# Kernel tuning notes

Measured on AMD Instinct MI355X. Metric: run time of the kernel, lower is better.

## Reference

```python
import jax, jax.numpy as jnp
import numpy as np
import math

DIM = 1024
HEADS = 16
DIM_HEAD = 64
INNER = HEADS * DIM_HEAD
NUM_BUCKETS = 32
MAX_DISTANCE = 128


def setup_inputs() -> dict:
    key = jax.random.key(0)
    ks = jax.random.split(key, 6)
    x = jax.random.normal(ks[0], (2, 2048, DIM), dtype=jnp.float32)
    Wq = jax.random.normal(ks[1], (DIM, INNER), dtype=jnp.float32) * (DIM ** -0.5)
    Wkv = jax.random.normal(ks[2], (DIM, 2 * DIM_HEAD), dtype=jnp.float32) * (DIM ** -0.5)
    Wout = jax.random.normal(ks[3], (INNER, DIM), dtype=jnp.float32) * (INNER ** -0.5)
    bout = jnp.zeros((DIM,), dtype=jnp.float32)
    rel_emb = jax.random.normal(ks[4], (NUM_BUCKETS, HEADS), dtype=jnp.float32) * 0.02
    return {"x": x, "Wq": Wq, "Wkv": Wkv, "Wout": Wout, "bout": bout, "rel_emb": rel_emb}


def _relative_position_bucket(rel_pos, num_buckets=NUM_BUCKETS, max_distance=MAX_DISTANCE):
    # rel_pos: [i, j] int32, k_pos - q_pos
    n = jnp.maximum(-rel_pos, 0)
    max_exact = num_buckets // 2
    is_small = n < max_exact
    n_safe = jnp.maximum(n, 1)  # avoid log(0); masked by is_small anyway
    val_if_large = max_exact + (
        jnp.log(n_safe.astype(jnp.float32) / max_exact)
        / math.log(max_distance / max_exact)
        * (num_buckets - max_exact)
    ).astype(jnp.int32)
    val_if_large = jnp.minimum(val_if_large, num_buckets - 1)
    return jnp.where(is_small, n, val_if_large)


def reference(x, Wq, Wkv, Wout, bout, rel_emb):
    b, n, _ = x.shape
    scale = DIM_HEAD ** -0.5
    bias_scale = DIM_HEAD ** 0.5

    q = (x @ Wq).reshape(b, n, HEADS, DIM_HEAD).transpose(0, 2, 1, 3) * scale  # [b,h,n,d]
    kv = x @ Wkv  # [b,n,2d]
    k, v = kv[..., :DIM_HEAD], kv[..., DIM_HEAD:]  # shared single-head K/V [b,n,d]

    sim = jnp.einsum('bhid,bjd->bhij', q, k)

    # T5 relative position bias
    pos = jnp.arange(n, dtype=jnp.int32)
    rel_pos = pos[None, :] - pos[:, None]  # [i,j] = k_pos - q_pos
    rp_bucket = _relative_position_bucket(rel_pos)
    bias = rel_emb[rp_bucket]  # [i,j,h]
    sim = sim + jnp.transpose(bias, (2, 0, 1))[None] * bias_scale

    # causal mask: mask strictly-upper triangle
    causal_mask = jnp.triu(jnp.ones((n, n), dtype=bool), k=1)
    neg = jnp.finfo(sim.dtype).max
    sim = jnp.where(causal_mask[None, None], -neg, sim)

    attn = jax.nn.softmax(sim, axis=-1)
    out = jnp.einsum('bhij,bjd->bhid', attn, v)
    out = out.transpose(0, 2, 1, 3).reshape(b, n, INNER)
    return out @ Wout + bout
```

## Files before the change

kernel.cpp:

```cpp
#include <hip/hip_runtime.h>
#include <cstdint>
#include <cmath>

typedef _Float16 half8 __attribute__((ext_vector_type(8)));
typedef unsigned short ushort8 __attribute__((ext_vector_type(8)));
typedef float floatx4 __attribute__((ext_vector_type(4)));

#define VT_STRIDE 2080

__device__ __forceinline__ unsigned short f2h(float f) {
    union { _Float16 h; unsigned short u; } cv;
    cv.h = (_Float16)f;
    return cv.u;
}

__device__ __forceinline__ void gld_lds16(const unsigned short* g, unsigned short* l) {
    __builtin_amdgcn_global_load_lds(
        (const __attribute__((address_space(1))) unsigned int*)g,
        (__attribute__((address_space(3))) unsigned int*)l, 16, 0, 0);
}

__global__ void cast_x_kernel(const float* __restrict__ x, unsigned short* __restrict__ xh, int n8) {
    int idx = blockIdx.x * blockDim.x + threadIdx.x;
    if (idx >= n8) return;
    const float4* p = (const float4*)x;
    float4 a = p[idx * 2], b = p[idx * 2 + 1];
    ushort8 o;
    o[0] = f2h(a.x); o[1] = f2h(a.y); o[2] = f2h(a.z); o[3] = f2h(a.w);
    o[4] = f2h(b.x); o[5] = f2h(b.y); o[6] = f2h(b.z); o[7] = f2h(b.w);
    *(ushort8*)(xh + (size_t)idx * 8) = o;
}

__global__ void transpose_fused_kernel(const float* __restrict__ Wq, const float* __restrict__ Wkv,
                                       const float* __restrict__ Wout,
                                       unsigned short* __restrict__ Wqkvt, unsigned short* __restrict__ Wot) {
    __shared__ float tile[32][33];
    int bxi = blockIdx.x;
    const float* in; unsigned short* out; int C; int cb;
    if (bxi < 32)      { in = Wq;   out = Wqkvt;                 C = 1024; cb = bxi; }
    else if (bxi < 36) { in = Wkv;  out = Wqkvt + 1024 * 1024;   C = 128;  cb = bxi - 32; }
    else               { in = Wout; out = Wot;                   C = 1024; cb = bxi - 36; }
    int bx = cb * 32, by = blockIdx.y * 32;
    int x = threadIdx.x, y0 = threadIdx.y;
    #pragma unroll
    for (int k = 0; k < 4; k++) {
        int y = y0 + k * 8;
        tile[y][x] = in[(size_t)(by + y) * C + bx + x];
    }
    __syncthreads();
    #pragma unroll
    for (int k = 0; k < 4; k++) {
        int y = y0 + k * 8;
        out[(size_t)(bx + y) * 1024 + by + x] = f2h(tile[x][y]);
    }
}

template<int MODE>
__global__ __launch_bounds__(256) void gemm_mn(
    const unsigned short* __restrict__ A, const unsigned short* __restrict__ Bt,
    unsigned short* __restrict__ oq, unsigned short* __restrict__ ok,
    unsigned short* __restrict__ ov, float* __restrict__ of,
    const float* __restrict__ bias)
{
    __shared__ __align__(16) unsigned short As[2][128 * 64];
    __shared__ __align__(16) unsigned short Bs[2][128 * 64];
    const int K = 1024;
    int t = threadIdx.x;
    int w = t >> 6, lane = t & 63, g = lane >> 4, il = lane & 15;
    int wr = w >> 1, wc = w & 1;
    int m0 = blockIdx.y * 128, n0 = blockIdx.x * 128;

    int l8 = lane >> 3, b8 = lane & 7;
    int swz = (b8 ^ l8) * 8;
    const unsigned short* Ag = A  + (size_t)(m0 + w * 32 + l8) * K + swz;
    const unsigned short* Bg = Bt + (size_t)(n0 + w * 32 + l8) * K + swz;
    int e0 = (g ^ (il & 7)) * 8;

    floatx4 acc[4][4] = {};

    #pragma unroll
    for (int q = 0; q < 4; q++) {
        gld_lds16(Ag + (size_t)(q * 8) * K, &As[0][(w * 32 + q * 8) * 64]);
        gld_lds16(Bg + (size_t)(q * 8) * K, &Bs[0][(w * 32 + q * 8) * 64]);
    }

    int cb = 0;
    for (int k0 = 0; k0 < K; k0 += 64, cb ^= 1) {
        __syncthreads();
        if (k0 + 64 < K) {
            #pragma unroll
            for (int q = 0; q < 4; q++) {
                gld_lds16(Ag + (size_t)(q * 8) * K + k0 + 64, &As[cb ^ 1][(w * 32 + q * 8) * 64]);
                gld_lds16(Bg + (size_t)(q * 8) * K + k0 + 64, &Bs[cb ^ 1][(w * 32 + q * 8) * 64]);
            }
        }
        const unsigned short* Ac = &As[cb][0];
        const unsigned short* Bc = &Bs[cb][0];
        #pragma unroll
        for (int ks = 0; ks < 2; ks++) {
            half8 a[4];
            #pragma unroll
            for (int mt = 0; mt < 4; mt++)
                a[mt] = *(const half8*)&Ac[(wr * 64 + mt * 16 + il) * 64 + (e0 ^ (ks * 32))];
            #pragma unroll
            for (int nt = 0; nt < 4; nt++) {
                half8 b = *(const half8*)&Bc[(wc * 64 + nt * 16 + il) * 64 + (e0 ^ (ks * 32))];
                #pragma unroll
                for (int mt = 0; mt < 4; mt++)
                    acc[mt][nt] = __builtin_amdgcn_mfma_f32_16x16x32_f16(a[mt], b, acc[mt][nt], 0, 0, 0);
            }
        }
    }

    #pragma unroll
    for (int mt = 0; mt < 4; mt++) {
        #pragma unroll
        for (int nt = 0; nt < 4; nt++) {
            #pragma unroll
            for (int r = 0; r < 4; r++) {
                int row = m0 + wr * 64 + mt * 16 + 4 * g + r;
                int col = n0 + wc * 64 + nt * 16 + il;
                float v = acc[mt][nt][r];
                if (MODE == 0) {
                    if (col < 1024) {
                        int b = row >> 11, i = row & 2047, h = col >> 6, d = col & 63;
                        oq[(size_t)((b * 16 + h) * 2048 + i) * 64 + d] = f2h(v * 0.18033688011112042f);
                    } else if (col < 1088) {
                        ok[(size_t)row * 64 + (col - 1024)] = f2h(v);
                    } else {
                        int b = row >> 11, j = row & 2047;
                        ov[(size_t)((b << 6) + (col - 1088)) * VT_STRIDE + j] = f2h(v);
                    }
                } else {
                    of[(size_t)row * 1024 + col] = v + bias[col];
                }
            }
        }
    }
}

__global__ __launch_bounds__(256) void attn_kernel(
    const unsigned short* __restrict__ qh, const unsigned short* __restrict__ kh,
    const unsigned short* __restrict__ vt, const float* __restrict__ rel_emb,
    unsigned short* __restrict__ ob)
{
    __shared__ float bias_tab[256];
    __shared__ __align__(16) unsigned short Ks[2][64 * 64];
    __shared__ __align__(16) unsigned short Vs[64 * 64];
    __shared__ __align__(16) unsigned short Pl[64 * 72];

    int bx = 31 - blockIdx.y;
    int bh = blockIdx.x;
    int b = bh >> 4, h = bh & 15;
    int t = threadIdx.x;
    int w = t >> 6, lane = t & 63, g = lane >> 4, il = lane & 15;

    {
        int dlt = t;
        int bucket;
        if (dlt < 16) bucket = dlt;
        else {
            float lg = logf((float)dlt * 0.0625f) / 2.0794415416798357f;
            int vv = 16 + (int)(lg * 16.0f);
            bucket = vv < 31 ? vv : 31;
        }
        bias_tab[dlt] = rel_emb[bucket * 16 + h] * 11.541560327111708f;
    }
    float cb31 = rel_emb[31 * 16 + h] * 11.541560327111708f;

    const unsigned short* kbase = kh + (size_t)b * (2048 * 64);
    const unsigned short* vbase = vt + (size_t)b * (64 * VT_STRIDE);
    int prow = (w * 16 + il) * 72;

    int l8 = lane >> 3, b8 = lane & 7;
    int swz = (b8 ^ l8) * 8;
    const unsigned short* kg_base = kbase + (size_t)(w * 16 + l8) * 64 + swz;
    const unsigned short* vg_base = vbase + (size_t)(w * 16 + l8) * VT_STRIDE + swz;
    int e0 = (g ^ (il & 7)) * 8;

    int iw = bx * 64 + w * 16;
    int i_glob = iw + il;
    const unsigned short* qrow = qh + (size_t)(bh * 2048 + i_glob) * 64;
    half8 qf0 = *(const half8*)(qrow + g * 8);
    half8 qf1 = *(const half8*)(qrow + 32 + g * 8);
    floatx4 O[4] = {};
    float m_run = -1e30f, l_run = 0.0f;

    gld_lds16(kg_base,                 &Ks[0][(w * 16) * 64]);
    gld_lds16(kg_base + 8 * 64,        &Ks[0][(w * 16 + 8) * 64]);
    gld_lds16(vg_base,                 &Vs[(w * 16) * 64]);
    gld_lds16(vg_base + 8 * VT_STRIDE, &Vs[(w * 16 + 8) * 64]);

    for (int c = 0; c <= bx; c++) {
        __syncthreads();
        if (c < bx) {
            const unsigned short* kg = kg_base + (size_t)(c + 1) * 4096;
            unsigned short* kd = &Ks[(c + 1) & 1][0];
            gld_lds16(kg,          &kd[(w * 16) * 64]);
            gld_lds16(kg + 8 * 64, &kd[(w * 16 + 8) * 64]);
        }
        const unsigned short* Kc = &Ks[c & 1][0];
        int j0 = c * 64;

        floatx4 S[4] = {};
        #pragma unroll
        for (int jt = 0; jt < 4; jt++) {
            half8 k0 = *(const half8*)&Kc[jt * 1024 + il * 64 + e0];
            half8 k1 = *(const half8*)&Kc[jt * 1024 + il * 64 + (e0 ^ 32)];
            S[jt] = __builtin_amdgcn_mfma_f32_16x16x32_f16(k0, qf0, S[jt], 0, 0, 0);
            S[jt] = __builtin_amdgcn_mfma_f32_16x16x32_f16(k1, qf1, S[jt], 0, 0, 0);
        }
        half8 vf[8];
        #pragma unroll
        for (int ks = 0; ks < 2; ks++)
            #pragma unroll
            for (int dt = 0; dt < 4; dt++)
                vf[ks * 4 + dt] = *(const half8*)&Vs[dt * 1024 + il * 64 + (e0 ^ (ks * 32))];

        asm volatile("s_waitcnt lgkmcnt(0)" ::: "memory");
        __builtin_amdgcn_s_barrier();
        if (c < bx) {
            const unsigned short* vg = vg_base + (c + 1) * 64;
            gld_lds16(vg,                 &Vs[(w * 16) * 64]);
            gld_lds16(vg + 8 * VT_STRIDE, &Vs[(w * 16 + 8) * 64]);
        }

        float s[16];
        if (c + 3 <= bx) {
            #pragma unroll
            for (int q2 = 0; q2 < 16; q2++) s[q2] = S[q2 >> 2][q2 & 3] + cb31;
        } else if (c < bx) {
            #pragma unroll
            for (int jt = 0; jt < 4; jt++)
                #pragma unroll
                for (int r = 0; r < 4; r++)
                    s[jt * 4 + r] = S[jt][r] + bias_tab[i_glob - (j0 + jt * 16 + 4 * g + r)];
        } else {
            #pragma unroll
            for (int jt = 0; jt < 4; jt++) {
                #pragma unroll
                for (int r = 0; r < 4; r++) {
                    int delta = i_glob - (j0 + jt * 16 + 4 * g + r);
                    int di = delta > 0 ? delta : 0;
                    s[jt * 4 + r] = (delta >= 0) ? (S[jt][r] + bias_tab[di]) : -1e30f;
                }
            }
        }
        float m8[8];
        #pragma unroll
        for (int q2 = 0; q2 < 8; q2++) m8[q2] = fmaxf(s[q2], s[q2 + 8]);
        #pragma unroll
        for (int q2 = 0; q2 < 4; q2++) m8[q2] = fmaxf(m8[q2], m8[q2 + 4]);
        float mx = fmaxf(fmaxf(m8[0], m8[1]), fmaxf(m8[2], m8[3]));
        mx = fmaxf(mx, __shfl_xor(mx, 16));
        mx = fmaxf(mx, __shfl_xor(mx, 32));
        float m_new = fmaxf(m_run, mx);
        float alpha = __builtin_amdgcn_exp2f(m_run - m_new);
        float p[16];
        #pragma unroll
        for (int q2 = 0; q2 < 16; q2++) p[q2] = __builtin_amdgcn_exp2f(s[q2] - m_new);
        float ps[8];
        #pragma unroll
        for (int q2 = 0; q2 < 8; q2++) ps[q2] = p[q2] + p[q2 + 8];
        #pragma unroll
        for (int q2 = 0; q2 < 4; q2++) ps[q2] += ps[q2 + 4];
        float psum = (ps[0] + ps[1]) + (ps[2] + ps[3]);
        psum += __shfl_xor(psum, 16);
        psum += __shfl_xor(psum, 32);
        l_run = l_run * alpha + psum;
        m_run = m_new;
        float arow[4];
        #pragma unroll
        for (int r = 0; r < 4; r++) arow[r] = __shfl(alpha, 4 * g + r);
        #pragma unroll
        for (int dt = 0; dt < 4; dt++)
            #pragma unroll
            for (int r = 0; r < 4; r++) O[dt][r] *= arow[r];
        #pragma unroll
        for (int jt = 0; jt < 4; jt++) {
            uint2 u;
            u.x = (unsigned int)f2h(p[jt * 4 + 0]) | ((unsigned int)f2h(p[jt * 4 + 1]) << 16);
            u.y = (unsigned int)f2h(p[jt * 4 + 2]) | ((unsigned int)f2h(p[jt * 4 + 3]) << 16);
            *(uint2*)&Pl[prow + jt * 16 + 4 * g] = u;
        }
        #pragma unroll
        for (int ks = 0; ks < 2; ks++) {
            half8 pf = *(const half8*)&Pl[prow + ks * 32 + g * 8];
            #pragma unroll
            for (int dt = 0; dt < 4; dt++)
                O[dt] = __builtin_amdgcn_mfma_f32_16x16x32_f16(pf, vf[ks * 4 + dt], O[dt], 0, 0, 0);
        }
    }
    float inv[4];
    #pragma unroll
    for (int r = 0; r < 4; r++) inv[r] = 1.0f / __shfl(l_run, 4 * g + r);
    #pragma unroll
    for (int dt = 0; dt < 4; dt++) {
        #pragma unroll
        for (int r = 0; r < 4; r++) {
            int i = iw + 4 * g + r;
            int d = dt * 16 + il;
            ob[(size_t)(b * 2048 + i) * 1024 + h * 64 + d] = f2h(O[dt][r] * inv[r]);
        }
    }
}

extern "C" void kernel_launch(void* const* d_in, const int* in_sizes, int n_in,
                              void* d_out, int out_size, void* d_ws, size_t ws_size,
                              hipStream_t stream) {
    const float* x    = (const float*)d_in[0];
    const float* Wq   = (const float*)d_in[1];
    const float* Wkv  = (const float*)d_in[2];
    const float* Wout = (const float*)d_in[3];
    const float* bout = (const float*)d_in[4];
    const float* rel  = (const float*)d_in[5];
    float* out = (float*)d_out;

    unsigned short* ws    = (unsigned short*)d_ws;
    unsigned short* xh    = ws;
    unsigned short* qh    = xh + 4194304;
    unsigned short* kh    = qh + 4194304;
    unsigned short* vt    = kh + 262144;
    unsigned short* Wqkvt = vt + 2 * 64 * VT_STRIDE;
    unsigned short* Wot   = Wqkvt + 1179648;
    unsigned short* ob    = xh;

    cast_x_kernel<<<2048, 256, 0, stream>>>(x, xh, 524288);
    transpose_fused_kernel<<<dim3(68, 32), dim3(32, 8), 0, stream>>>(Wq, Wkv, Wout, Wqkvt, Wot);
    gemm_mn<0><<<dim3(9, 32), 256, 0, stream>>>(xh, Wqkvt, qh, kh, vt, nullptr, nullptr);
    attn_kernel<<<dim3(32, 32), 256, 0, stream>>>(qh, kh, vt, rel, ob);
    gemm_mn<2><<<dim3(8, 32), 256, 0, stream>>>(ob, Wot, nullptr, nullptr, nullptr, out, bout);
}
```

Measured before the change: 175.1 us.

## Shrink GEMM M-tile, reorder grid, tune waits, and skip redundant softmax rescales

The GEMM kernels move from 128x128 to 64x128 tiles with blockIdx.x walking M, which roughly doubles block count for better CU occupancy on the projection GEMMs. The double-buffer sync becomes explicit partial vmcnt waits plus raw barriers. In attention, the distant-bucket bias constant is folded out of the table (softmax shift invariance) so far tiles skip the add. The online-softmax rescale now runs only when some row max grows. Smaller tiles cut per-block reuse and add B-matrix traffic, and the hand-written waitcnt logic is fragile.

```diff
diff --git a/kernel.cpp b/kernel.cpp
--- a/kernel.cpp
+++ b/kernel.cpp
@@ -62,63 +62,72 @@
     unsigned short* __restrict__ ov, float* __restrict__ of,
     const float* __restrict__ bias)
 {
-    __shared__ __align__(16) unsigned short As[2][128 * 64];
+    __shared__ __align__(16) unsigned short As[2][64 * 64];
     __shared__ __align__(16) unsigned short Bs[2][128 * 64];
     const int K = 1024;
     int t = threadIdx.x;
     int w = t >> 6, lane = t & 63, g = lane >> 4, il = lane & 15;
     int wr = w >> 1, wc = w & 1;
-    int m0 = blockIdx.y * 128, n0 = blockIdx.x * 128;
+    int m0 = blockIdx.x * 64, n0 = blockIdx.y * 128;
 
     int l8 = lane >> 3, b8 = lane & 7;
     int swz = (b8 ^ l8) * 8;
-    const unsigned short* Ag = A  + (size_t)(m0 + w * 32 + l8) * K + swz;
+    const unsigned short* Ag = A  + (size_t)(m0 + w * 16 + l8) * K + swz;
     const unsigned short* Bg = Bt + (size_t)(n0 + w * 32 + l8) * K + swz;
     int e0 = (g ^ (il & 7)) * 8;
 
-    floatx4 acc[4][4] = {};
-
-    #pragma unroll
-    for (int q = 0; q < 4; q++) {
-        gld_lds16(Ag + (size_t)(q * 8) * K, &As[0][(w * 32 + q * 8) * 64]);
+    floatx4 acc[2][4] = {};
+
+    #pragma unroll
+    for (int q = 0; q < 2; q++)
+        gld_lds16(Ag + (size_t)(q * 8) * K, &As[0][(w * 16 + q * 8) * 64]);
+    #pragma unroll
+    for (int q = 0; q < 4; q++)
         gld_lds16(Bg + (size_t)(q * 8) * K, &Bs[0][(w * 32 + q * 8) * 64]);
-    }
 
     int cb = 0;
     for (int k0 = 0; k0 < K; k0 += 64, cb ^= 1) {
-        __syncthreads();
         if (k0 + 64 < K) {
             #pragma unroll
-            for (int q = 0; q < 4; q++) {
-                gld_lds16(Ag + (size_t)(q * 8) * K + k0 + 64, &As[cb ^ 1][(w * 32 + q * 8) * 64]);
+            for (int q = 0; q < 2; q++)
+                gld_lds16(Ag + (size_t)(q * 8) * K + k0 + 64, &As[cb ^ 1][(w * 16 + q * 8) * 64]);
+            #pragma unroll
+            for (int q = 0; q < 4; q++)
                 gld_lds16(Bg + (size_t)(q * 8) * K + k0 + 64, &Bs[cb ^ 1][(w * 32 + q * 8) * 64]);
-            }
-        }
+            asm volatile("s_waitcnt vmcnt(6)" ::: "memory");
+        } else {
+            asm volatile("s_waitcnt vmcnt(0)" ::: "memory");
+        }
+        __builtin_amdgcn_s_barrier();
+        __builtin_amdgcn_sched_barrier(0);
+
         const unsigned short* Ac = &As[cb][0];
         const unsigned short* Bc = &Bs[cb][0];
         #pragma unroll
         for (int ks = 0; ks < 2; ks++) {
-            half8 a[4];
-            #pragma unroll
-            for (int mt = 0; mt < 4; mt++)
-                a[mt] = *(const half8*)&Ac[(wr * 64 + mt * 16 + il) * 64 + (e0 ^ (ks * 32))];
+            half8 a[2];
+            #pragma unroll
+            for (int mt = 0; mt < 2; mt++)
+                a[mt] = *(const half8*)&Ac[(wr * 32 + mt * 16 + il) * 64 + (e0 ^ (ks * 32))];
             #pragma unroll
             for (int nt = 0; nt < 4; nt++) {
                 half8 b = *(const half8*)&Bc[(wc * 64 + nt * 16 + il) * 64 + (e0 ^ (ks * 32))];
                 #pragma unroll
-                for (int mt = 0; mt < 4; mt++)
+                for (int mt = 0; mt < 2; mt++)
                     acc[mt][nt] = __builtin_amdgcn_mfma_f32_16x16x32_f16(a[mt], b, acc[mt][nt], 0, 0, 0);
             }
         }
-    }
-
-    #pragma unroll
-    for (int mt = 0; mt < 4; mt++) {
+        asm volatile("s_waitcnt lgkmcnt(0)" ::: "memory");
+        __builtin_amdgcn_s_barrier();
+    }
+
+    #pragma unroll
+    for (int mt = 0; mt < 2; mt++) {
         #pragma unroll
         for (int nt = 0; nt < 4; nt++) {
             #pragma unroll
             for (int r = 0; r < 4; r++) {
-                int row = m0 + wr * 64 + mt * 16 + 4 * g + r;
+                int row = m0 + wr * 32 + mt * 16 + 4 * g + r;
                 int col = n0 + wc * 64 + nt * 16 + il;
                 float v = acc[mt][nt][r];
                 if (MODE == 0) {
@@ -155,6 +164,7 @@
     int t = threadIdx.x;
     int w = t >> 6, lane = t & 63, g = lane >> 4, il = lane & 15;
 
+    float cbv = rel_emb[31 * 16 + h];
     {
         int dlt = t;
         int bucket;
@@ -164,9 +174,8 @@
             int vv = 16 + (int)(lg * 16.0f);
             bucket = vv < 31 ? vv : 31;
         }
-        bias_tab[dlt] = rel_emb[bucket * 16 + h] * 11.541560327111708f;
-    }
-    float cb31 = rel_emb[31 * 16 + h] * 11.541560327111708f;
+        bias_tab[dlt] = (rel_emb[bucket * 16 + h] - cbv) * 11.541560327111708f;
+    }
 
     const unsigned short* kbase = kh + (size_t)b * (2048 * 64);
     const unsigned short* vbase = vt + (size_t)b * (64 * VT_STRIDE);
@@ -228,7 +237,7 @@
         float s[16];
         if (c + 3 <= bx) {
             #pragma unroll
-            for (int q2 = 0; q2 < 16; q2++) s[q2] = S[q2 >> 2][q2 & 3] + cb31;
+            for (int q2 = 0; q2 < 16; q2++) s[q2] = S[q2 >> 2][q2 & 3];
         } else if (c < bx) {
             #pragma unroll
             for (int jt = 0; jt < 4; jt++)
@@ -254,11 +263,22 @@
         float mx = fmaxf(fmaxf(m8[0], m8[1]), fmaxf(m8[2], m8[3]));
         mx = fmaxf(mx, __shfl_xor(mx, 16));
         mx = fmaxf(mx, __shfl_xor(mx, 32));
-        float m_new = fmaxf(m_run, mx);
-        float alpha = __builtin_amdgcn_exp2f(m_run - m_new);
+        if (__any(mx > m_run)) {
+            float m_new = fmaxf(m_run, mx);
+            float alpha = __builtin_amdgcn_exp2f(m_run - m_new);
+            l_run *= alpha;
+            float arow[4];
+            #pragma unroll
+            for (int r = 0; r < 4; r++) arow[r] = __shfl(alpha, 4 * g + r);
+            #pragma unroll
+            for (int dt = 0; dt < 4; dt++)
+                #pragma unroll
+                for (int r = 0; r < 4; r++) O[dt][r] *= arow[r];
+            m_run = m_new;
+        }
         float p[16];
         #pragma unroll
-        for (int q2 = 0; q2 < 16; q2++) p[q2] = __builtin_amdgcn_exp2f(s[q2] - m_new);
+        for (int q2 = 0; q2 < 16; q2++) p[q2] = __builtin_amdgcn_exp2f(s[q2] - m_run);
         float ps[8];
         #pragma unroll
         for (int q2 = 0; q2 < 8; q2++) ps[q2] = p[q2] + p[q2 + 8];
@@ -267,15 +287,8 @@
         float psum = (ps[0] + ps[1]) + (ps[2] + ps[3]);
         psum += __shfl_xor(psum, 16);
         psum += __shfl_xor(psum, 32);
-        l_run = l_run * alpha + psum;
-        m_run = m_new;
-        float arow[4];
-        #pragma unroll
-        for (int r = 0; r < 4; r++) arow[r] = __shfl(alpha, 4 * g + r);
-        #pragma unroll
-        for (int dt = 0; dt < 4; dt++)
-            #pragma unroll
-            for (int r = 0; r < 4; r++) O[dt][r] *= arow[r];
+        l_run += psum;
+
         #pragma unroll
         for (int jt = 0; jt < 4; jt++) {
             uint2 u;
@@ -327,7 +340,7 @@
 
     cast_x_kernel<<<2048, 256, 0, stream>>>(x, xh, 524288);
     transpose_fused_kernel<<<dim3(68, 32), dim3(32, 8), 0, stream>>>(Wq, Wkv, Wout, Wqkvt, Wot);
-    gemm_mn<0><<<dim3(9, 32), 256, 0, stream>>>(xh, Wqkvt, qh, kh, vt, nullptr, nullptr);
+    gemm_mn<0><<<dim3(64, 9), 256, 0, stream>>>(xh, Wqkvt, qh, kh, vt, nullptr, nullptr);
     attn_kernel<<<dim3(32, 32), 256, 0, stream>>>(qh, kh, vt, rel, ob);
-    gemm_mn<2><<<dim3(8, 32), 256, 0, stream>>>(ob, Wot, nullptr, nullptr, nullptr, out, bout);
-}
+    gemm_mn<2><<<dim3(64, 8), 256, 0, stream>>>(ob, Wot, nullptr, nullptr, nullptr, out, bout);
+}
```

Result: faster. 167.1 us (-4.6%).
